# Kernel optimization log

Measured on AMD Instinct MI355X. Metric: run time of the kernel, lower is better.

The kernel has to match this reference:

```python
import jax, jax.numpy as jnp
import numpy as np

B, L, D, H = 4, 2048, 512, 8
HD = D // H  # 64
MAX_REL = 4


def setup_inputs() -> dict:
    key = jax.random.key(0)
    ks = jax.random.split(key, 13)
    s = 1.0 / np.sqrt(D)
    return {
        "q": jax.random.normal(ks[0], (B, L, D), jnp.float32),
        "k": jax.random.normal(ks[1], (B, L, D), jnp.float32),
        "v": jax.random.normal(ks[2], (B, L, D), jnp.float32),
        "Wq": jax.random.normal(ks[3], (D, D), jnp.float32) * s,
        "bq": jax.random.normal(ks[4], (D,), jnp.float32) * 0.01,
        "Wk": jax.random.normal(ks[5], (D, D), jnp.float32) * s,
        "bk": jax.random.normal(ks[6], (D,), jnp.float32) * 0.01,
        "Wv": jax.random.normal(ks[7], (D, D), jnp.float32) * s,
        "bv": jax.random.normal(ks[8], (D,), jnp.float32) * 0.01,
        "Wo": jax.random.normal(ks[9], (D, D), jnp.float32) * s,
        "bo": jax.random.normal(ks[10], (D,), jnp.float32) * 0.01,
        "rel_k_table": jax.random.normal(ks[11], (2 * MAX_REL + 1, HD), jnp.float32),
        "rel_v_table": jax.random.normal(ks[12], (2 * MAX_REL + 1, HD), jnp.float32),
    }


def _to_heads(x):
    # [B, L, D] -> [B, H, L, HD]
    b, l, d = x.shape
    return x.reshape(b, l, H, d // H).transpose(0, 2, 1, 3)


def reference(q, k, v, Wq, bq, Wk, bk, Wv, bv, Wo, bo, rel_k_table, rel_v_table):
    # NOTE: in the source, the relative-attention output is overwritten by the
    # plain SDPA call immediately after, so observable math = SDPA only.
    # rel_k_table / rel_v_table are dead parameters (zero gradient).
    relu = jax.nn.relu
    qh = _to_heads(relu(q @ Wq.T + bq))  # [B,H,L,HD]
    kh = _to_heads(relu(k @ Wk.T + bk))
    vh = _to_heads(relu(v @ Wv.T + bv))
    # scale by sqrt(d_key)=sqrt(512), matching the original (not sqrt(head_dim))
    scores = jnp.einsum("bhqd,bhkd->bhqk", qh, kh) / jnp.sqrt(jnp.float32(D))
    attn = jax.nn.softmax(scores, axis=-1)
    out = jnp.einsum("bhqk,bhkd->bhqd", attn, vh)  # [B,H,L,HD]
    out = out.transpose(0, 2, 1, 3).reshape(B, L, D)
    return relu(out @ Wo.T + bo)
```

## Files before the change

### kernel.cpp

```cpp
#include <hip/hip_runtime.h>
#include <hip/hip_bf16.h>

#define B_  4
#define L_  2048
#define D_  512
#define H_  8
#define HD_ 64
#define M_  (B_ * L_)

typedef __bf16 bf16;
typedef __attribute__((ext_vector_type(8)))  __bf16 bf16x8;
typedef __attribute__((ext_vector_type(4)))  __bf16 bf16x4;
typedef __attribute__((ext_vector_type(16))) float  f32x16;

__device__ __forceinline__ f32x16 mfma32(bf16x8 a, bf16x8 b, f32x16 c) {
    return __builtin_amdgcn_mfma_f32_32x32x16_bf16(a, b, c, 0, 0, 0);
}

__device__ __forceinline__ void pack_body(const float* __restrict__ src,
                                          bf16* __restrict__ dst, int R,
                                          int m0, int k0)
{
    __shared__ __align__(16) bf16 tile[64][76];
    const int t = threadIdx.x;
#pragma unroll
    for (int rep = 0; rep < 4; rep++) {
        const int idx = rep * 256 + t;
        const int r = idx >> 4, c4 = idx & 15;
        const float4 f = *(const float4*)(src + (size_t)(m0 + r) * 512 + k0 + c4 * 4);
        bf16x4 v; v[0] = (bf16)f.x; v[1] = (bf16)f.y; v[2] = (bf16)f.z; v[3] = (bf16)f.w;
        *(bf16x4*)(&tile[r][c4 * 4]) = v;
    }
    __syncthreads();
#pragma unroll
    for (int rep = 0; rep < 2; rep++) {
        const int s = rep * 256 + t;
        const int ml = s & 63, kpl = s >> 6;
        const bf16x4 lo = *(const bf16x4*)(&tile[ml][kpl * 8]);
        const bf16x4 hi4 = *(const bf16x4*)(&tile[ml][kpl * 8 + 4]);
        bf16x8 v;
#pragma unroll
        for (int e = 0; e < 4; e++) { v[e] = lo[e]; v[e + 4] = hi4[e]; }
        *(bf16x8*)(dst + ((size_t)(k0 / 8 + kpl) * R + m0 + ml) * 8) = v;
    }
}

__global__ __launch_bounds__(256) void pack_w(
    const float* __restrict__ W0, const float* __restrict__ W1,
    const float* __restrict__ W2, const float* __restrict__ W3,
    bf16* __restrict__ Wp)
{
    const int z = blockIdx.z;
    const float* src = z == 0 ? W0 : z == 1 ? W1 : z == 2 ? W2 : W3;
    pack_body(src, Wp + (size_t)z * 64 * 512 * 8, 512, blockIdx.x * 64, blockIdx.y * 64);
}

struct PJob {
    const bf16* X; const float* Xf; const bf16* W; const float* bias;
    void* out; float postmul; int mode;
};

__device__ __forceinline__ void barrier_lds_only()
{
    asm volatile("s_waitcnt lgkmcnt(0)" ::: "memory");
    __builtin_amdgcn_s_barrier();
}

__device__ __forceinline__ void proj_epilogue_elem(const PJob& jb, int row,
                                                   int col, float v)
{
    const int mode = jb.mode;
    if (mode == 2) {
        ((float*)jb.out)[(size_t)row * D_ + col] = v;
    } else {
        v *= jb.postmul;
        const int b = row >> 11, l = row & (L_ - 1);
        const int h = col >> 6,  hd = col & (HD_ - 1);
        const int bh = b * H_ + h;
        size_t idx;
        if (mode == 0) {
            idx = ((size_t)bh * L_ + l) * HD_ + hd;
        } else if (mode == 1) {
            idx = (((size_t)bh * 8 + (hd >> 3)) * L_ + l) * 8 + (hd & 7);
        } else {
            const int swzl = (l & ~15) | (l & 3) | ((l & 4) << 1) | ((l & 8) >> 1);
            idx = (((size_t)bh * 256 + (swzl >> 3)) * 64 + hd) * 8 + (swzl & 7);
        }
        ((bf16*)jb.out)[idx] = (bf16)v;
    }
}

__global__ __launch_bounds__(256, 3) void proj_qkv_kernel(PJob j0, PJob j1, PJob j2)
{
    const PJob jb = (blockIdx.z == 0) ? j0 : (blockIdx.z == 1) ? j1 : j2;
    const int w    = threadIdx.x >> 6;
    const int lane = threadIdx.x & 63;
    const int l31  = lane & 31;
    const int hi   = lane >> 5;
    const int m0 = blockIdx.x * 128;
    const int n0 = blockIdx.y * 128;
    const int mh = w & 1;
    const int nh = w >> 1;

    __shared__ __align__(16) bf16 Ab[2][8][64][8];
    __shared__ __align__(16) bf16 Bb[2][8][64][8];

    f32x16 acc[2][2];
#pragma unroll
    for (int mi = 0; mi < 2; mi++)
#pragma unroll
        for (int ni = 0; ni < 2; ni++)
#pragma unroll
            for (int r = 0; r < 16; r++) acc[mi][ni][r] = 0.0f;

    auto ldB = [&](int f, int k0) -> bf16x8 {
        return *(const bf16x8*)(jb.W + ((size_t)((k0 >> 3) + (f >> 2) * 2 + hi) * 512
                                        + n0 + (f & 3) * 32 + l31) * 8);
    };

    bf16x8 rB[2][2];
    float4 rT[2][4];

    auto ldT = [&](int s, int k0) {
#pragma unroll
        for (int rep = 0; rep < 4; rep++) {
            const int idx = rep * 256 + (int)threadIdx.x;
            rT[s][rep] = *(const float4*)(jb.Xf + (size_t)(m0 + (idx >> 3)) * 512
                                          + k0 + (idx & 7) * 4);
        }
    };
    auto stA = [&](int s, int buf) {
#pragma unroll
        for (int rep = 0; rep < 4; rep++) {
            const int idx = rep * 256 + (int)threadIdx.x;
            const int r = idx >> 3, c4 = idx & 7;
            const float4 f = rT[s][rep];
            bf16x4 v; v[0] = (bf16)f.x; v[1] = (bf16)f.y;
            v[2] = (bf16)f.z; v[3] = (bf16)f.w;
            const int fs = ((c4 >> 2) << 2) | (r >> 5);
            const int ln = (r & 31) | (((c4 >> 1) & 1) << 5);
            *(bf16x4*)(&Ab[buf][fs][ln][(c4 & 1) * 4]) = v;
        }
    };

    ldT(0, 0); stA(0, 0); ldT(1, 32); ldT(0, 64);
#pragma unroll
    for (int i = 0; i < 2; i++) rB[0][i] = ldB(w * 2 + i, 0);
#pragma unroll
    for (int i = 0; i < 2; i++)
        *(bf16x8*)(&Bb[0][w * 2 + i][lane][0]) = rB[0][i];
#pragma unroll
    for (int i = 0; i < 2; i++) rB[1][i] = ldB(w * 2 + i, 32);
#pragma unroll
    for (int i = 0; i < 2; i++) rB[0][i] = ldB(w * 2 + i, 64);
    __syncthreads();

#pragma unroll
    for (int it = 0; it < 16; it++) {
        const int cur = it & 1;
#pragma unroll
        for (int ks = 0; ks < 2; ks++) {
            const bf16x8 a0 = *(const bf16x8*)(&Ab[cur][ks * 4 + mh * 2 + 0][lane][0]);
            const bf16x8 a1 = *(const bf16x8*)(&Ab[cur][ks * 4 + mh * 2 + 1][lane][0]);
            const bf16x8 b0 = *(const bf16x8*)(&Bb[cur][ks * 4 + nh * 2 + 0][lane][0]);
            const bf16x8 b1 = *(const bf16x8*)(&Bb[cur][ks * 4 + nh * 2 + 1][lane][0]);
            acc[0][0] = mfma32(a0, b0, acc[0][0]);
            acc[0][1] = mfma32(a0, b1, acc[0][1]);
            acc[1][0] = mfma32(a1, b0, acc[1][0]);
            acc[1][1] = mfma32(a1, b1, acc[1][1]);
        }
        if (it < 15) {
            const int s = (it + 1) & 1;
            stA(s, 1 - cur);
#pragma unroll
            for (int i = 0; i < 2; i++)
                *(bf16x8*)(&Bb[1 - cur][w * 2 + i][lane][0]) = rB[s][i];
            if (it < 13) {
                ldT(s, (it + 3) * 32);
#pragma unroll
                for (int i = 0; i < 2; i++)
                    rB[s][i] = ldB(w * 2 + i, (it + 3) * 32);
            }
            barrier_lds_only();
        }
    }

#pragma unroll
    for (int ni = 0; ni < 2; ni++) {
        const int col = n0 + (nh * 2 + ni) * 32 + l31;
        const float bn = jb.bias[col];
#pragma unroll
        for (int mi = 0; mi < 2; mi++)
#pragma unroll
            for (int r = 0; r < 16; r++) {
                const int row = m0 + (mh * 2 + mi) * 32 + (r & 3) + 8 * (r >> 2) + 4 * hi;
                proj_epilogue_elem(jb, row, col, fmaxf(acc[mi][ni][r] + bn, 0.0f));
            }
    }
}

__global__ __launch_bounds__(256, 3) void proj_o_kernel(PJob jb)
{
    const int w    = threadIdx.x >> 6;
    const int lane = threadIdx.x & 63;
    const int l31  = lane & 31;
    const int hi   = lane >> 5;
    const int m0 = blockIdx.x * 128;
    const int n0 = blockIdx.y * 64;
    const int mh = w & 1;
    const int nh = w >> 1;

    __shared__ __align__(16) bf16 Ab[2][16][64][8];
    __shared__ __align__(16) bf16 Bb[2][8][64][8];

    f32x16 acc[2];
#pragma unroll
    for (int mi = 0; mi < 2; mi++)
#pragma unroll
        for (int r = 0; r < 16; r++) acc[mi][r] = 0.0f;

    auto ldA = [&](int f, int k0) -> bf16x8 {
        return *(const bf16x8*)(jb.X + ((size_t)((k0 >> 3) + (f >> 2) * 2 + hi) * M_
                                        + m0 + (f & 3) * 32 + l31) * 8);
    };
    auto ldB = [&](int f, int k0) -> bf16x8 {
        return *(const bf16x8*)(jb.W + ((size_t)((k0 >> 3) + (f >> 1) * 2 + hi) * 512
                                        + n0 + (f & 1) * 32 + l31) * 8);
    };

    bf16x8 rA[3][4], rB[3][2];
#pragma unroll
    for (int i = 0; i < 4; i++) rA[0][i] = ldA(w * 4 + i, 0);
#pragma unroll
    for (int i = 0; i < 2; i++) rB[0][i] = ldB(w * 2 + i, 0);
#pragma unroll
    for (int i = 0; i < 4; i++) *(bf16x8*)(&Ab[0][w * 4 + i][lane][0]) = rA[0][i];
#pragma unroll
    for (int i = 0; i < 2; i++) *(bf16x8*)(&Bb[0][w * 2 + i][lane][0]) = rB[0][i];
#pragma unroll
    for (int s = 1; s < 3; s++) {
#pragma unroll
        for (int i = 0; i < 4; i++) rA[s][i] = ldA(w * 4 + i, s * 64);
#pragma unroll
        for (int i = 0; i < 2; i++) rB[s][i] = ldB(w * 2 + i, s * 64);
    }
    __syncthreads();

#pragma unroll
    for (int it = 0; it < 8; it++) {
        const int cur = it & 1;
        if (it < 5) {
            const int s = it % 3, kn = (it + 3) * 64;
#pragma unroll
            for (int i = 0; i < 4; i++) rA[s][i] = ldA(w * 4 + i, kn);
#pragma unroll
            for (int i = 0; i < 2; i++) rB[s][i] = ldB(w * 2 + i, kn);
        }
#pragma unroll
        for (int ks = 0; ks < 4; ks++) {
            const bf16x8 bfr = *(const bf16x8*)(&Bb[cur][ks * 2 + nh][lane][0]);
#pragma unroll
            for (int mi = 0; mi < 2; mi++) {
                const bf16x8 afr = *(const bf16x8*)(&Ab[cur][ks * 4 + mh * 2 + mi][lane][0]);
                acc[mi] = mfma32(afr, bfr, acc[mi]);
            }
        }
        if (it < 7) {
            const int s = (it + 1) % 3;
#pragma unroll
            for (int i = 0; i < 4; i++) *(bf16x8*)(&Ab[1 - cur][w * 4 + i][lane][0]) = rA[s][i];
#pragma unroll
            for (int i = 0; i < 2; i++) *(bf16x8*)(&Bb[1 - cur][w * 2 + i][lane][0]) = rB[s][i];
            __syncthreads();
        }
    }

    const int col = n0 + nh * 32 + l31;
    const float bn = jb.bias[col];
#pragma unroll
    for (int mi = 0; mi < 2; mi++)
#pragma unroll
        for (int r = 0; r < 16; r++) {
            const int row = m0 + (mh * 2 + mi) * 32 + (r & 3) + 8 * (r >> 2) + 4 * hi;
            proj_epilogue_elem(jb, row, col, fmaxf(acc[mi][r] + bn, 0.0f));
        }
}

__global__ __launch_bounds__(128, 2) void attn_kernel(
    const bf16* __restrict__ qh, const bf16* __restrict__ Kp,
    const bf16* __restrict__ Vp, bf16* __restrict__ Op)
{
    const int w    = threadIdx.x >> 6;
    const int lane = threadIdx.x & 63;
    const int l31  = lane & 31;
    const int hi   = lane >> 5;

    const int lin  = blockIdx.x + (blockIdx.y << 5);
    const int xcd  = lin & 7;
    const int slot = lin >> 3;
    const int bh   = (xcd << 2) + (slot >> 5);
    const int qb   = (slot & 31) * 64 + w * 32;

    const bf16* Q   = qh + (size_t)bh * L_ * HD_;
    const bf16* Kpb = Kp + (size_t)bh * 8 * L_ * 8;
    const bf16* Vpb = Vp + (size_t)bh * 256 * 64 * 8;

    __shared__ __align__(16) bf16 Vb[2][8][64][8];

    bf16x8 qf[4];
#pragma unroll
    for (int ks = 0; ks < 4; ks++)
        qf[ks] = *(const bf16x8*)(Q + (size_t)(qb + l31) * HD_ + ks * 16 + hi * 8);

    f32x16 zz;
#pragma unroll
    for (int r = 0; r < 16; r++) zz[r] = 0.0f;
    f32x16 o0 = zz, o1 = zz, lacc = zz;
    bf16x8 ones;
#pragma unroll
    for (int u = 0; u < 8; u++) ones[u] = (bf16)1.0f;

    auto ldK = [&](int f, int t) -> bf16x8 {
        return *(const bf16x8*)(Kpb + ((size_t)((f >> 1) * 2 + hi) * L_
                                       + t * 64 + (f & 1) * 32 + l31) * 8);
    };
    auto ldV = [&](int f, int t) -> bf16x8 {
        return *(const bf16x8*)(Vpb + ((size_t)(t * 8 + (f >> 1) * 2 + hi) * 64
                                       + (f & 1) * 32 + l31) * 8);
    };

    bf16x8 kr[8], vr[2][4];
#pragma unroll
    for (int i = 0; i < 4; i++) vr[0][i] = ldV(w * 4 + i, 0);
#pragma unroll
    for (int i = 0; i < 4; i++) *(bf16x8*)(&Vb[0][w * 4 + i][lane][0]) = vr[0][i];
#pragma unroll
    for (int i = 0; i < 4; i++) vr[1][i] = ldV(w * 4 + i, 1);
#pragma unroll
    for (int i = 0; i < 4; i++) vr[0][i] = ldV(w * 4 + i, 2);
#pragma unroll
    for (int f = 0; f < 8; f++) kr[f] = ldK(f, 0);
    __syncthreads();

    auto tile_body = [&](int t, int cur, int nxt) {
        f32x16 s0 = mfma32(kr[0], qf[0], zz);
        f32x16 s1 = mfma32(kr[1], qf[0], zz);
#pragma unroll
        for (int ks = 1; ks < 4; ks++) {
            s0 = mfma32(kr[ks * 2 + 0], qf[ks], s0);
            s1 = mfma32(kr[ks * 2 + 1], qf[ks], s1);
        }
        if (t < 31) {
#pragma unroll
            for (int f = 0; f < 8; f++) kr[f] = ldK(f, t + 1);
        }

#pragma unroll
        for (int r = 0; r < 16; r++) s0[r] = __builtin_amdgcn_exp2f(s0[r]);
        {
            bf16x8 pf0, pf1;
#pragma unroll
            for (int u = 0; u < 8; u++) { pf0[u] = (bf16)s0[u]; pf1[u] = (bf16)s0[8 + u]; }
            o0   = mfma32(pf0, *(const bf16x8*)(&Vb[cur][0][lane][0]), o0);
            o1   = mfma32(pf0, *(const bf16x8*)(&Vb[cur][1][lane][0]), o1);
            lacc = mfma32(pf0, ones, lacc);
            o0   = mfma32(pf1, *(const bf16x8*)(&Vb[cur][2][lane][0]), o0);
            o1   = mfma32(pf1, *(const bf16x8*)(&Vb[cur][3][lane][0]), o1);
            lacc = mfma32(pf1, ones, lacc);
        }
#pragma unroll
        for (int r = 0; r < 16; r++) s1[r] = __builtin_amdgcn_exp2f(s1[r]);
        {
            bf16x8 pf2, pf3;
#pragma unroll
            for (int u = 0; u < 8; u++) { pf2[u] = (bf16)s1[u]; pf3[u] = (bf16)s1[8 + u]; }
            o0   = mfma32(pf2, *(const bf16x8*)(&Vb[cur][4][lane][0]), o0);
            o1   = mfma32(pf2, *(const bf16x8*)(&Vb[cur][5][lane][0]), o1);
            lacc = mfma32(pf2, ones, lacc);
            o0   = mfma32(pf3, *(const bf16x8*)(&Vb[cur][6][lane][0]), o0);
            o1   = mfma32(pf3, *(const bf16x8*)(&Vb[cur][7][lane][0]), o1);
            lacc = mfma32(pf3, ones, lacc);
        }

        if (t < 31) {
#pragma unroll
            for (int i = 0; i < 4; i++)
                *(bf16x8*)(&Vb[1 - cur][w * 4 + i][lane][0]) = vr[nxt][i];
            const int tn = (t + 3 < 32) ? t + 3 : 31;
#pragma unroll
            for (int i = 0; i < 4; i++) vr[nxt][i] = ldV(w * 4 + i, tn);
            __syncthreads();
        }
    };

    for (int tt = 0; tt < 16; tt++) {
        tile_body(2 * tt + 0, 0, 1);
        tile_body(2 * tt + 1, 1, 0);
    }

    const int b = bh >> 3, h = bh & 7;
#pragma unroll
    for (int r = 0; r < 16; r++) {
        const int rl = (r & 3) + 8 * (r >> 2) + 4 * hi;
        const float inv = 1.0f / lacc[r];
        const int m = b * L_ + qb + rl;
        const int c0 = h * HD_ + l31;
        Op[((size_t)(c0 >> 3) * M_ + m) * 8 + (c0 & 7)] = (bf16)(o0[r] * inv);
        const int c1 = c0 + 32;
        Op[((size_t)(c1 >> 3) * M_ + m) * 8 + (c1 & 7)] = (bf16)(o1[r] * inv);
    }
}

extern "C" void kernel_launch(void* const* d_in, const int* in_sizes, int n_in,
                              void* d_out, int out_size, void* d_ws, size_t ws_size,
                              hipStream_t stream)
{
    (void)in_sizes; (void)n_in; (void)out_size; (void)ws_size;
    const float* q  = (const float*)d_in[0];
    const float* k  = (const float*)d_in[1];
    const float* v  = (const float*)d_in[2];
    const float* Wq = (const float*)d_in[3];
    const float* bq = (const float*)d_in[4];
    const float* Wk = (const float*)d_in[5];
    const float* bk = (const float*)d_in[6];
    const float* Wv = (const float*)d_in[7];
    const float* bv = (const float*)d_in[8];
    const float* Wo = (const float*)d_in[9];
    const float* bo = (const float*)d_in[10];
    float* out = (float*)d_out;

    char* ws = (char*)d_ws;
    const size_t MB = 1024 * 1024;
    bf16* Vp  = (bf16*)(ws);
    bf16* Opb = (bf16*)(ws + 8 * MB);
    bf16* Wp  = (bf16*)(ws + 16 * MB);
    bf16* qh  = (bf16*)(d_out);
    bf16* Kp  = (bf16*)((char*)d_out + 8 * MB);

    bf16* Wqp = Wp;
    bf16* Wkp = Wp + (size_t)64 * 512 * 8;
    bf16* Wvp = Wp + (size_t)2 * 64 * 512 * 8;
    bf16* Wop = Wp + (size_t)3 * 64 * 512 * 8;

    const float SCALE_LOG2E = 0.06377946282349575f;

    pack_w<<<dim3(8, 8, 4), dim3(256), 0, stream>>>(Wq, Wk, Wv, Wo, Wp);

    PJob jq{nullptr, q, Wqp, bq, qh, SCALE_LOG2E, 0};
    PJob jk{nullptr, k, Wkp, bk, Kp, 1.0f, 1};
    PJob jv{nullptr, v, Wvp, bv, Vp, 1.0f, 3};
    proj_qkv_kernel<<<dim3(64, 4, 3), dim3(256), 0, stream>>>(jq, jk, jv);

    attn_kernel<<<dim3(32, 32), dim3(128), 0, stream>>>(qh, Kp, Vp, Opb);

    PJob jo{Opb, nullptr, Wop, bo, out, 1.0f, 2};
    proj_o_kernel<<<dim3(64, 8), dim3(256), 0, stream>>>(jo);
}
```

Measured before the change: 191.5 us.

## Fuse weight fp32-to-bf16 packing into projection GEMM tile loads

Removes the separate pack_w kernel that converted and repacked all four weight matrices to bf16. The QKV and output projection kernels now load fp32 weight tiles directly, convert them in registers and store them into the swizzled LDS layout, the same way the activations are handled. This saves one kernel launch and a round trip through global memory for the packed weights. In exchange, each block re-reads and re-converts fp32 weights (twice the bytes of bf16) and uses more registers for staging.

```diff
diff --git a/kernel.cpp b/kernel.cpp
--- a/kernel.cpp
+++ b/kernel.cpp
@@ -17,46 +17,8 @@
     return __builtin_amdgcn_mfma_f32_32x32x16_bf16(a, b, c, 0, 0, 0);
 }
 
-__device__ __forceinline__ void pack_body(const float* __restrict__ src,
-                                          bf16* __restrict__ dst, int R,
-                                          int m0, int k0)
-{
-    __shared__ __align__(16) bf16 tile[64][76];
-    const int t = threadIdx.x;
-#pragma unroll
-    for (int rep = 0; rep < 4; rep++) {
-        const int idx = rep * 256 + t;
-        const int r = idx >> 4, c4 = idx & 15;
-        const float4 f = *(const float4*)(src + (size_t)(m0 + r) * 512 + k0 + c4 * 4);
-        bf16x4 v; v[0] = (bf16)f.x; v[1] = (bf16)f.y; v[2] = (bf16)f.z; v[3] = (bf16)f.w;
-        *(bf16x4*)(&tile[r][c4 * 4]) = v;
-    }
-    __syncthreads();
-#pragma unroll
-    for (int rep = 0; rep < 2; rep++) {
-        const int s = rep * 256 + t;
-        const int ml = s & 63, kpl = s >> 6;
-        const bf16x4 lo = *(const bf16x4*)(&tile[ml][kpl * 8]);
-        const bf16x4 hi4 = *(const bf16x4*)(&tile[ml][kpl * 8 + 4]);
-        bf16x8 v;
-#pragma unroll
-        for (int e = 0; e < 4; e++) { v[e] = lo[e]; v[e + 4] = hi4[e]; }
-        *(bf16x8*)(dst + ((size_t)(k0 / 8 + kpl) * R + m0 + ml) * 8) = v;
-    }
-}
-
-__global__ __launch_bounds__(256) void pack_w(
-    const float* __restrict__ W0, const float* __restrict__ W1,
-    const float* __restrict__ W2, const float* __restrict__ W3,
-    bf16* __restrict__ Wp)
-{
-    const int z = blockIdx.z;
-    const float* src = z == 0 ? W0 : z == 1 ? W1 : z == 2 ? W2 : W3;
-    pack_body(src, Wp + (size_t)z * 64 * 512 * 8, 512, blockIdx.x * 64, blockIdx.y * 64);
-}
-
 struct PJob {
-    const bf16* X; const float* Xf; const bf16* W; const float* bias;
+    const bf16* X; const float* Xf; const float* Wf; const float* bias;
     void* out; float postmul; int mode;
 };
 
@@ -93,8 +55,8 @@
 __global__ __launch_bounds__(256, 3) void proj_qkv_kernel(PJob j0, PJob j1, PJob j2)
 {
     const PJob jb = (blockIdx.z == 0) ? j0 : (blockIdx.z == 1) ? j1 : j2;
+    const int lane = threadIdx.x & 63;
     const int w    = threadIdx.x >> 6;
-    const int lane = threadIdx.x & 63;
     const int l31  = lane & 31;
     const int hi   = lane >> 5;
     const int m0 = blockIdx.x * 128;
@@ -113,46 +75,34 @@
 #pragma unroll
             for (int r = 0; r < 16; r++) acc[mi][ni][r] = 0.0f;
 
-    auto ldB = [&](int f, int k0) -> bf16x8 {
-        return *(const bf16x8*)(jb.W + ((size_t)((k0 >> 3) + (f >> 2) * 2 + hi) * 512
-                                        + n0 + (f & 3) * 32 + l31) * 8);
-    };
-
-    bf16x8 rB[2][2];
-    float4 rT[2][4];
-
-    auto ldT = [&](int s, int k0) {
+    float4 rT[2][4], rTB[2][4];
+
+    auto ldT = [&](float4 (&rr)[2][4], const float* src, int base, int s, int k0) {
 #pragma unroll
         for (int rep = 0; rep < 4; rep++) {
             const int idx = rep * 256 + (int)threadIdx.x;
-            rT[s][rep] = *(const float4*)(jb.Xf + (size_t)(m0 + (idx >> 3)) * 512
+            rr[s][rep] = *(const float4*)(src + (size_t)(base + (idx >> 3)) * 512
                                           + k0 + (idx & 7) * 4);
         }
     };
-    auto stA = [&](int s, int buf) {
+    auto stT = [&](const float4 (&rr)[2][4], bf16 (*dst)[64][8], int s) {
 #pragma unroll
         for (int rep = 0; rep < 4; rep++) {
             const int idx = rep * 256 + (int)threadIdx.x;
             const int r = idx >> 3, c4 = idx & 7;
-            const float4 f = rT[s][rep];
+            const float4 f = rr[s][rep];
             bf16x4 v; v[0] = (bf16)f.x; v[1] = (bf16)f.y;
             v[2] = (bf16)f.z; v[3] = (bf16)f.w;
             const int fs = ((c4 >> 2) << 2) | (r >> 5);
             const int ln = (r & 31) | (((c4 >> 1) & 1) << 5);
-            *(bf16x4*)(&Ab[buf][fs][ln][(c4 & 1) * 4]) = v;
-        }
-    };
-
-    ldT(0, 0); stA(0, 0); ldT(1, 32); ldT(0, 64);
-#pragma unroll
-    for (int i = 0; i < 2; i++) rB[0][i] = ldB(w * 2 + i, 0);
-#pragma unroll
-    for (int i = 0; i < 2; i++)
-        *(bf16x8*)(&Bb[0][w * 2 + i][lane][0]) = rB[0][i];
-#pragma unroll
-    for (int i = 0; i < 2; i++) rB[1][i] = ldB(w * 2 + i, 32);
-#pragma unroll
-    for (int i = 0; i < 2; i++) rB[0][i] = ldB(w * 2 + i, 64);
+            *(bf16x4*)(&dst[fs][ln][(c4 & 1) * 4]) = v;
+        }
+    };
+
+    ldT(rT, jb.Xf, m0, 0, 0);  ldT(rTB, jb.Wf, n0, 0, 0);
+    stT(rT, Ab[0], 0);         stT(rTB, Bb[0], 0);
+    ldT(rT, jb.Xf, m0, 1, 32); ldT(rTB, jb.Wf, n0, 1, 32);
+    ldT(rT, jb.Xf, m0, 0, 64); ldT(rTB, jb.Wf, n0, 0, 64);
     __syncthreads();
 
 #pragma unroll
@@ -171,15 +121,11 @@
         }
         if (it < 15) {
             const int s = (it + 1) & 1;
-            stA(s, 1 - cur);
-#pragma unroll
-            for (int i = 0; i < 2; i++)
-                *(bf16x8*)(&Bb[1 - cur][w * 2 + i][lane][0]) = rB[s][i];
+            stT(rT, Ab[1 - cur], s);
+            stT(rTB, Bb[1 - cur], s);
             if (it < 13) {
-                ldT(s, (it + 3) * 32);
-#pragma unroll
-                for (int i = 0; i < 2; i++)
-                    rB[s][i] = ldB(w * 2 + i, (it + 3) * 32);
+                ldT(rT, jb.Xf, m0, s, (it + 3) * 32);
+                ldT(rTB, jb.Wf, n0, s, (it + 3) * 32);
             }
             barrier_lds_only();
         }
@@ -223,27 +169,44 @@
         return *(const bf16x8*)(jb.X + ((size_t)((k0 >> 3) + (f >> 2) * 2 + hi) * M_
                                         + m0 + (f & 3) * 32 + l31) * 8);
     };
-    auto ldB = [&](int f, int k0) -> bf16x8 {
-        return *(const bf16x8*)(jb.W + ((size_t)((k0 >> 3) + (f >> 1) * 2 + hi) * 512
-                                        + n0 + (f & 1) * 32 + l31) * 8);
-    };
-
-    bf16x8 rA[3][4], rB[3][2];
+
+    bf16x8 rA[3][4];
+    float4 rTB[2][4];
+
+    auto ldTB = [&](int s, int k0) {
+#pragma unroll
+        for (int rep = 0; rep < 4; rep++) {
+            const int idx = rep * 256 + (int)threadIdx.x;
+            rTB[s][rep] = *(const float4*)(jb.Wf + (size_t)(n0 + (idx >> 4)) * 512
+                                           + k0 + (idx & 15) * 4);
+        }
+    };
+    auto stTB = [&](int s, int buf) {
+#pragma unroll
+        for (int rep = 0; rep < 4; rep++) {
+            const int idx = rep * 256 + (int)threadIdx.x;
+            const int r = idx >> 4, c4 = idx & 15;
+            const float4 f = rTB[s][rep];
+            bf16x4 v; v[0] = (bf16)f.x; v[1] = (bf16)f.y;
+            v[2] = (bf16)f.z; v[3] = (bf16)f.w;
+            const int fs = ((c4 >> 2) << 1) | (r >> 5);
+            const int ln = (r & 31) | (((c4 >> 1) & 1) << 5);
+            *(bf16x4*)(&Bb[buf][fs][ln][(c4 & 1) * 4]) = v;
+        }
+    };
+
 #pragma unroll
     for (int i = 0; i < 4; i++) rA[0][i] = ldA(w * 4 + i, 0);
-#pragma unroll
-    for (int i = 0; i < 2; i++) rB[0][i] = ldB(w * 2 + i, 0);
+    ldTB(0, 0);
 #pragma unroll
     for (int i = 0; i < 4; i++) *(bf16x8*)(&Ab[0][w * 4 + i][lane][0]) = rA[0][i];
-#pragma unroll
-    for (int i = 0; i < 2; i++) *(bf16x8*)(&Bb[0][w * 2 + i][lane][0]) = rB[0][i];
-#pragma unroll
-    for (int s = 1; s < 3; s++) {
+    stTB(0, 0);
+#pragma unroll
+    for (int s = 1; s < 3; s++)
 #pragma unroll
         for (int i = 0; i < 4; i++) rA[s][i] = ldA(w * 4 + i, s * 64);
-#pragma unroll
-        for (int i = 0; i < 2; i++) rB[s][i] = ldB(w * 2 + i, s * 64);
-    }
+    ldTB(1, 64);
+    ldTB(0, 128);
     __syncthreads();
 
 #pragma unroll
@@ -253,8 +216,6 @@
             const int s = it % 3, kn = (it + 3) * 64;
 #pragma unroll
             for (int i = 0; i < 4; i++) rA[s][i] = ldA(w * 4 + i, kn);
-#pragma unroll
-            for (int i = 0; i < 2; i++) rB[s][i] = ldB(w * 2 + i, kn);
         }
 #pragma unroll
         for (int ks = 0; ks < 4; ks++) {
@@ -266,11 +227,12 @@
             }
         }
         if (it < 7) {
-            const int s = (it + 1) % 3;
-#pragma unroll
-            for (int i = 0; i < 4; i++) *(bf16x8*)(&Ab[1 - cur][w * 4 + i][lane][0]) = rA[s][i];
-#pragma unroll
-            for (int i = 0; i < 2; i++) *(bf16x8*)(&Bb[1 - cur][w * 2 + i][lane][0]) = rB[s][i];
+            const int sA = (it + 1) % 3;
+#pragma unroll
+            for (int i = 0; i < 4; i++) *(bf16x8*)(&Ab[1 - cur][w * 4 + i][lane][0]) = rA[sA][i];
+            const int sB = (it + 1) & 1;
+            stTB(sB, 1 - cur);
+            if (it < 5) ldTB(sB, (it + 3) * 64);
             __syncthreads();
         }
     }
@@ -433,26 +395,18 @@
     const size_t MB = 1024 * 1024;
     bf16* Vp  = (bf16*)(ws);
     bf16* Opb = (bf16*)(ws + 8 * MB);
-    bf16* Wp  = (bf16*)(ws + 16 * MB);
     bf16* qh  = (bf16*)(d_out);
     bf16* Kp  = (bf16*)((char*)d_out + 8 * MB);
 
-    bf16* Wqp = Wp;
-    bf16* Wkp = Wp + (size_t)64 * 512 * 8;
-    bf16* Wvp = Wp + (size_t)2 * 64 * 512 * 8;
-    bf16* Wop = Wp + (size_t)3 * 64 * 512 * 8;
-
     const float SCALE_LOG2E = 0.06377946282349575f;
 
-    pack_w<<<dim3(8, 8, 4), dim3(256), 0, stream>>>(Wq, Wk, Wv, Wo, Wp);
-
-    PJob jq{nullptr, q, Wqp, bq, qh, SCALE_LOG2E, 0};
-    PJob jk{nullptr, k, Wkp, bk, Kp, 1.0f, 1};
-    PJob jv{nullptr, v, Wvp, bv, Vp, 1.0f, 3};
+    PJob jq{nullptr, q, Wq, bq, qh, SCALE_LOG2E, 0};
+    PJob jk{nullptr, k, Wk, bk, Kp, 1.0f, 1};
+    PJob jv{nullptr, v, Wv, bv, Vp, 1.0f, 3};
     proj_qkv_kernel<<<dim3(64, 4, 3), dim3(256), 0, stream>>>(jq, jk, jv);
 
     attn_kernel<<<dim3(32, 32), dim3(128), 0, stream>>>(qh, Kp, Vp, Opb);
 
-    PJob jo{Opb, nullptr, Wop, bo, out, 1.0f, 2};
+    PJob jo{Opb, nullptr, Wo, bo, out, 1.0f, 2};
     proj_o_kernel<<<dim3(64, 8), dim3(256), 0, stream>>>(jo);
 }
```

Result: slower. 198.4 us (+3.6%).
